# Optimization experiments

Measured on AMD Instinct MI355X. Metric: run time of the kernel, lower is better.

Reference implementation:

```python
import jax, jax.numpy as jnp
import numpy as np

TOP_K = 4
NUM_EXPERTS = 128
HIDDEN_DIM = 2880


def setup_inputs() -> dict:
    key = jax.random.key(0)
    k1, k2, k3 = jax.random.split(key, 3)
    hidden_states = jax.random.normal(k1, (4, 4096, HIDDEN_DIM), dtype=jnp.float32)
    weight = jax.random.normal(k2, (NUM_EXPERTS, HIDDEN_DIM), dtype=jnp.float32) * 0.02
    bias = jax.random.normal(k3, (NUM_EXPERTS,), dtype=jnp.float32) * 0.02
    return {"hidden_states": hidden_states, "weight": weight, "bias": bias}


def reference(hidden_states, weight, bias):
    # flatten tokens: [T, H]
    h = hidden_states.reshape(-1, HIDDEN_DIM)
    # router logits: [T, E]
    router_logits = jnp.einsum("th,eh->te", h, weight) + bias
    # top-k over experts
    router_top_value, router_indices = jax.lax.top_k(router_logits, TOP_K)  # [T, K]
    # softmax over the k selected logits only
    router_top_value = jax.nn.softmax(router_top_value, axis=-1)
    # scatter softmaxed weights back into dense [T, E] score matrix
    T = router_logits.shape[0]
    rows = jnp.arange(T)[:, None]  # [T, 1] broadcast against [T, K]
    router_scores = jnp.zeros_like(router_logits).at[rows, router_indices].set(router_top_value)
    # histogram of expert selections
    expert_select_count = jnp.zeros((NUM_EXPERTS,), dtype=jnp.int32).at[router_indices.reshape(-1)].add(
        jnp.ones((T * TOP_K,), dtype=jnp.int32)
    )
    return router_scores, router_indices, expert_select_count
```

## Files before the change

kernel.cpp:

```cpp
#include <hip/hip_runtime.h>
#include <math.h>

#define HID 2880
#define NE  128
#define BK  64
#define TOKB 64
#define NCH 45
#define HN  15
#define PSTR 129

typedef _Float16 half4v __attribute__((ext_vector_type(4)));
typedef _Float16 half8v __attribute__((ext_vector_type(8)));
typedef float    f32x4v __attribute__((ext_vector_type(4)));

__global__ __launch_bounds__(256)
void prep_w(const float* __restrict__ W, _Float16* __restrict__ whi,
            _Float16* __restrict__ wlo)
{
    const int e = blockIdx.x;
    for (int j = 0; j < 12; ++j) {
        const int k = j * 256 + threadIdx.x;
        if (k >= HID) break;
        const float v = W[(size_t)e * HID + k];
        const _Float16 h = (_Float16)v;
        const _Float16 l = (_Float16)(v - (float)h);
        const size_t idx = (size_t)(k >> 6) * 8192 + ((k >> 5) & 1) * 4096
                         + e * 32 + (k & 31);
        whi[idx] = h;
        wlo[idx] = l;
    }
}

#define GLOAD(dst, ptr) \
    asm volatile("global_load_dwordx4 %0, %1, off" : "=v"(dst) : "v"(ptr))

__global__ __launch_bounds__(768, 1)
void fused_router(const float* __restrict__ A, const _Float16* __restrict__ whi,
                  const _Float16* __restrict__ wlo, const float* __restrict__ bias,
                  float* __restrict__ scores, float* __restrict__ idxOut,
                  float* __restrict__ counts)
{
    __shared__ __align__(16) char smem[98304];
    __shared__ float sval[TOKB][4];
    __shared__ int   sidx[TOKB][4];
    __shared__ int   hist[NE];

#define SA(ks, buf, h, sub) \
    (smem + (ks) * 32768 + ((((buf) * 2 + (h)) * 2 + (sub)) * 4096))

#define SWZ(tok) ((((tok) >> 1) & 3) << 4)

    const int tid  = threadIdx.x;
    const int lane = tid & 63;
    const int wv   = __builtin_amdgcn_readfirstlane(tid >> 6);
    const int ks   = wv >> 2;
    const int wq   = wv & 3;
    const int lg   = lane >> 4;
    const int lr   = lane & 15;
    const int tokBase = blockIdx.x * TOKB;
    const int hbeg = ks * HN;

    const _Float16* wHp[2];
    const _Float16* wLp[2];
#pragma unroll
    for (int m = 0; m < 2; ++m) {
        const size_t b = (size_t)((wq * 32 + m * 16 + lr) * 32 + lg * 8);
        wHp[m] = whi + b;
        wLp[m] = wlo + b;
    }

    const int gid = tid & 255;
    const float* aSrcP[4];
    int aSub[4], aWr[4];
#pragma unroll
    for (int p = 0; p < 4; ++p) {
        const int f = p * 256 + gid;
        const int tok = f >> 4, sl = f & 15;
        aSub[p] = sl >> 3;
        const int q = sl & 7;
        aSrcP[p] = A + (size_t)(tokBase + tok) * HID + aSub[p] * 32 + q * 4;
        aWr[p] = tok * 64 + ((q * 8) ^ SWZ(tok));
    }

    int aRd[4];
#pragma unroll
    for (int n = 0; n < 4; ++n) {
        const int tok = n * 16 + lr;
        aRd[n] = tok * 64 + ((lg * 16) ^ SWZ(tok));
    }

    float4 aA, aB, aC, aD;
#define AISSUE(c) do {                                                         \
    GLOAD(aA, aSrcP[0] + (size_t)(c) * BK);                                    \
    GLOAD(aB, aSrcP[1] + (size_t)(c) * BK);                                    \
    GLOAD(aC, aSrcP[2] + (size_t)(c) * BK);                                    \
    GLOAD(aD, aSrcP[3] + (size_t)(c) * BK);                                    \
} while (0)

#define WISSUE(SET, c) do {                                                    \
    _Pragma("unroll")                                                          \
    for (int m = 0; m < 2; ++m)                                                \
        _Pragma("unroll")                                                      \
        for (int s = 0; s < 2; ++s) {                                          \
            const size_t o = (size_t)(c) * 8192 + s * 4096;                    \
            GLOAD(SET[m * 4 + s * 2 + 0], wHp[m] + o);                         \
            GLOAD(SET[m * 4 + s * 2 + 1], wLp[m] + o);                         \
        }                                                                      \
} while (0)

    auto CONVA = [&](int buf) {
#pragma unroll
        for (int p = 0; p < 4; ++p) {
            const float4 v = (p == 0) ? aA : (p == 1) ? aB : (p == 2) ? aC : aD;
            const _Float16 h0 = (_Float16)v.x, h1 = (_Float16)v.y,
                           h2 = (_Float16)v.z, h3 = (_Float16)v.w;
            const half4v hh = {h0, h1, h2, h3};
            const half4v ll = {(_Float16)(v.x - (float)h0),
                               (_Float16)(v.y - (float)h1),
                               (_Float16)(v.z - (float)h2),
                               (_Float16)(v.w - (float)h3)};
            *reinterpret_cast<half4v*>(SA(ks, buf, 0, aSub[p]) + aWr[p]) = hh;
            *reinterpret_cast<half4v*>(SA(ks, buf, 1, aSub[p]) + aWr[p]) = ll;
        }
    };

    f32x4v acc[2][4];
#pragma unroll
    for (int m = 0; m < 2; ++m)
#pragma unroll
        for (int n = 0; n < 4; ++n) acc[m][n] = (f32x4v)0.f;

    half8v wA[8], wB[8];

#define STEP(i, SU, SF) do {                                                   \
    if ((i) + 1 < HN) { AISSUE(hbeg + (i) + 1); WISSUE(SF, hbeg + (i) + 1); }  \
    __builtin_amdgcn_sched_barrier(0);                                         \
    if ((i) + 1 < HN) asm volatile("s_waitcnt vmcnt(12)" ::: "memory");        \
    else              asm volatile("s_waitcnt vmcnt(0)" ::: "memory");         \
    __builtin_amdgcn_sched_barrier(0);                                         \
    const int buf_ = (i) & 1;                                                  \
    _Pragma("unroll")                                                          \
    for (int s = 0; s < 2; ++s)                                                \
        _Pragma("unroll")                                                      \
        for (int n = 0; n < 4; ++n) {                                          \
            const half8v ah = *reinterpret_cast<const half8v*>(                \
                SA(ks, buf_, 0, s) + aRd[n]);                                  \
            const half8v al = *reinterpret_cast<const half8v*>(                \
                SA(ks, buf_, 1, s) + aRd[n]);                                  \
            _Pragma("unroll")                                                  \
            for (int m = 0; m < 2; ++m) {                                      \
                acc[m][n] = __builtin_amdgcn_mfma_f32_16x16x32_f16(            \
                    SU[m * 4 + s * 2 + 0], ah, acc[m][n], 0, 0, 0);            \
                acc[m][n] = __builtin_amdgcn_mfma_f32_16x16x32_f16(            \
                    SU[m * 4 + s * 2 + 1], ah, acc[m][n], 0, 0, 0);            \
                acc[m][n] = __builtin_amdgcn_mfma_f32_16x16x32_f16(            \
                    SU[m * 4 + s * 2 + 0], al, acc[m][n], 0, 0, 0);            \
            }                                                                  \
        }                                                                      \
    if ((i) + 1 < HN) {                                                        \
        asm volatile("s_waitcnt vmcnt(8)" ::: "memory");                       \
        __builtin_amdgcn_sched_barrier(0);                                     \
        CONVA(((i) + 1) & 1);                                                  \
    }                                                                          \
    asm volatile("s_waitcnt lgkmcnt(0)" ::: "memory");                         \
    __builtin_amdgcn_sched_barrier(0);                                         \
    __builtin_amdgcn_s_barrier();                                              \
    __builtin_amdgcn_sched_barrier(0);                                         \
} while (0)

    AISSUE(hbeg);
    WISSUE(wA, hbeg);
    asm volatile("s_waitcnt vmcnt(8)" ::: "memory");
    __builtin_amdgcn_sched_barrier(0);
    CONVA(0);
    asm volatile("s_waitcnt lgkmcnt(0)" ::: "memory");
    __builtin_amdgcn_sched_barrier(0);
    __builtin_amdgcn_s_barrier();
    __builtin_amdgcn_sched_barrier(0);

#pragma unroll 1
    for (int i = 0; i < HN - 1; i += 2) {
        STEP(i,     wA, wB);
        STEP(i + 1, wB, wA);
    }
    STEP(HN - 1, wA, wB);

    float* P1   = (float*)(smem);
    float* P2   = (float*)(smem + 33024);
    float* cval = (float*)(smem + 66048);
    int*   cidx = (int*)(smem + 74496);

    if (tid < NE) hist[tid] = 0;

    if (ks == 1 || ks == 2) {
        float* P = (ks == 1) ? P1 : P2;
#pragma unroll
        for (int m = 0; m < 2; ++m)
#pragma unroll
            for (int n = 0; n < 4; ++n)
#pragma unroll
                for (int r = 0; r < 4; ++r) {
                    const int e = wq * 32 + m * 16 + lg * 4 + r;
                    const int t = n * 16 + lr;
                    P[t * PSTR + e] = acc[m][n][r];
                }
    }
    __syncthreads();

    if (ks == 0) {
#pragma unroll
        for (int m = 0; m < 2; ++m)
#pragma unroll
            for (int n = 0; n < 4; ++n)
#pragma unroll
                for (int r = 0; r < 4; ++r) {
                    const int e = wq * 32 + m * 16 + lg * 4 + r;
                    const int t = n * 16 + lr;
                    const int off = t * PSTR + e;
                    P1[off] = ((acc[m][n][r] + P1[off]) + P2[off]) + bias[e];
                }
    }
    __syncthreads();

    if (tid < 512) {
        const int t = tid & 63, g = tid >> 6;
        float v0 = -1e30f, v1 = -1e30f, v2 = -1e30f, v3 = -1e30f;
        int   i0 = 0, i1 = 0, i2 = 0, i3 = 0;
        const int e0 = g * 16;
#pragma unroll 4
        for (int i = 0; i < 16; ++i) {
            const int e = e0 + i;
            const float v = P1[t * PSTR + e];
            if (v > v3) {
                if (v > v2) {
                    v3 = v2; i3 = i2;
                    if (v > v1) {
                        v2 = v1; i2 = i1;
                        if (v > v0) { v1 = v0; i1 = i0; v0 = v; i0 = e; }
                        else        { v1 = v;  i1 = e; }
                    } else { v2 = v; i2 = e; }
                } else { v3 = v; i3 = e; }
            }
        }
        cval[t * 33 + g * 4 + 0] = v0; cidx[t * 33 + g * 4 + 0] = i0;
        cval[t * 33 + g * 4 + 1] = v1; cidx[t * 33 + g * 4 + 1] = i1;
        cval[t * 33 + g * 4 + 2] = v2; cidx[t * 33 + g * 4 + 2] = i2;
        cval[t * 33 + g * 4 + 3] = v3; cidx[t * 33 + g * 4 + 3] = i3;
    }
    __syncthreads();

    if (tid < TOKB) {
        const int t = tid;
        float m0 = -1e30f, m1 = -1e30f, m2 = -1e30f, m3 = -1e30f;
        int   j0 = 0, j1 = 0, j2 = 0, j3 = 0;
#pragma unroll
        for (int q = 0; q < 32; ++q) {
            const float v = cval[t * 33 + q];
            const int   e = cidx[t * 33 + q];
            if (v > m3) {
                if (v > m2) {
                    m3 = m2; j3 = j2;
                    if (v > m1) {
                        m2 = m1; j2 = j1;
                        if (v > m0) { m1 = m0; j1 = j0; m0 = v; j0 = e; }
                        else        { m1 = v;  j1 = e; }
                    } else { m2 = v; j2 = e; }
                } else { m3 = v; j3 = e; }
            }
        }
        const float x1 = expf(m1 - m0), x2 = expf(m2 - m0), x3 = expf(m3 - m0);
        const float inv = 1.f / (1.f + x1 + x2 + x3);
        sval[t][0] = inv;      sidx[t][0] = j0;
        sval[t][1] = x1 * inv; sidx[t][1] = j1;
        sval[t][2] = x2 * inv; sidx[t][2] = j2;
        sval[t][3] = x3 * inv; sidx[t][3] = j3;
        atomicAdd(&hist[j0], 1); atomicAdd(&hist[j1], 1);
        atomicAdd(&hist[j2], 1); atomicAdd(&hist[j3], 1);
    }
    __syncthreads();

    const size_t sBase = (size_t)blockIdx.x * TOKB * NE;
#pragma unroll 4
    for (int it = 0; it < 11; ++it) {
        const int flat = it * 768 + tid;
        if (flat < TOKB * NE) {
            const int t = flat >> 7, e = flat & 127;
            float val = 0.f;
            val = (e == sidx[t][0]) ? sval[t][0] : val;
            val = (e == sidx[t][1]) ? sval[t][1] : val;
            val = (e == sidx[t][2]) ? sval[t][2] : val;
            val = (e == sidx[t][3]) ? sval[t][3] : val;
            scores[sBase + flat] = val;
        }
    }
    if (tid < TOKB * 4)
        idxOut[(size_t)blockIdx.x * TOKB * 4 + tid] =
            (float)sidx[tid >> 2][tid & 3];
    if (tid < NE) {
        const int c = hist[tid];
        if (c) atomicAdd(&counts[tid], (float)c);
    }
#undef SA
#undef SWZ
#undef AISSUE
#undef WISSUE
#undef STEP
}

extern "C" void kernel_launch(void* const* d_in, const int* in_sizes, int n_in,
                              void* d_out, int out_size, void* d_ws, size_t ws_size,
                              hipStream_t stream) {
    const float* A = (const float*)d_in[0];
    const float* W = (const float*)d_in[1];
    const float* B = (const float*)d_in[2];
    const int T = in_sizes[0] / HID;

    float* out = (float*)d_out;
    float* scores = out;
    float* idxOut = out + (size_t)T * NE;
    float* counts = idxOut + (size_t)T * 4;

    _Float16* whi = (_Float16*)d_ws;
    _Float16* wlo = whi + (size_t)NE * HID;

    hipMemsetAsync(counts, 0, NE * sizeof(float), stream);

    hipLaunchKernelGGL(prep_w, dim3(NE), dim3(256), 0, stream, W, whi, wlo);
    hipLaunchKernelGGL(fused_router, dim3(T / TOKB), dim3(768), 0, stream,
                       A, whi, wlo, B, scores, idxOut, counts);
}
```

Measured before the change: 65.38 us.

## Halve token and K tiles to cut LDS and registers for multi-block occupancy

Reduces the per-block token tile from 64 to 32 and the K chunk from 64 to 32. This shrinks shared memory from about 96KB to about 41KB and halves the accumulator and weight register sets, and launch bounds now request 6 blocks per CU instead of 1. The load pipeline, address math, vmcnt thresholds, LDS layout and top-k/scatter loops are all reworked to match. The intent is more resident blocks and waves to hide memory latency and to spread 512 blocks instead of 256 across CUs. The cost is that every weight chunk is reloaded twice as often per token, and each step carries more pipeline and synchronisation overhead.

```diff
diff --git a/kernel.cpp b/kernel.cpp
--- a/kernel.cpp
+++ b/kernel.cpp
@@ -3,10 +3,10 @@
 
 #define HID 2880
 #define NE  128
-#define BK  64
-#define TOKB 64
-#define NCH 45
-#define HN  15
+#define BK  32
+#define TOKB 32
+#define NCH 90
+#define HN  30
 #define PSTR 129
 
 typedef _Float16 half4v __attribute__((ext_vector_type(4)));
@@ -33,20 +33,22 @@
 
 #define GLOAD(dst, ptr) \
     asm volatile("global_load_dwordx4 %0, %1, off" : "=v"(dst) : "v"(ptr))
-
-__global__ __launch_bounds__(768, 1)
+#define GLOAD_O1024(dst, ptr) \
+    asm volatile("global_load_dwordx4 %0, %1, off offset:1024" : "=v"(dst) : "v"(ptr))
+
+__global__ __launch_bounds__(768, 6)
 void fused_router(const float* __restrict__ A, const _Float16* __restrict__ whi,
                   const _Float16* __restrict__ wlo, const float* __restrict__ bias,
                   float* __restrict__ scores, float* __restrict__ idxOut,
                   float* __restrict__ counts)
 {
-    __shared__ __align__(16) char smem[98304];
+    __shared__ __align__(16) char smem[41472];
     __shared__ float sval[TOKB][4];
     __shared__ int   sidx[TOKB][4];
     __shared__ int   hist[NE];
 
-#define SA(ks, buf, h, sub) \
-    (smem + (ks) * 32768 + ((((buf) * 2 + (h)) * 2 + (sub)) * 4096))
+#define SA(ks, buf, h) \
+    (smem + (ks) * 8192 + (((buf) * 2 + (h)) * 2048))
 
 #define SWZ(tok) ((((tok) >> 1) & 3) << 4)
 
@@ -60,105 +62,79 @@
     const int tokBase = blockIdx.x * TOKB;
     const int hbeg = ks * HN;
 
-    const _Float16* wHp[2];
-    const _Float16* wLp[2];
-#pragma unroll
-    for (int m = 0; m < 2; ++m) {
-        const size_t b = (size_t)((wq * 32 + m * 16 + lr) * 32 + lg * 8);
-        wHp[m] = whi + b;
-        wLp[m] = wlo + b;
-    }
+    const _Float16* wHp0 = whi + (size_t)((wq * 32 + lr) * 32 + lg * 8);
+    const _Float16* wLp0 = wlo + (size_t)((wq * 32 + lr) * 32 + lg * 8);
 
     const int gid = tid & 255;
-    const float* aSrcP[4];
-    int aSub[4], aWr[4];
-#pragma unroll
-    for (int p = 0; p < 4; ++p) {
-        const int f = p * 256 + gid;
-        const int tok = f >> 4, sl = f & 15;
-        aSub[p] = sl >> 3;
-        const int q = sl & 7;
-        aSrcP[p] = A + (size_t)(tokBase + tok) * HID + aSub[p] * 32 + q * 4;
-        aWr[p] = tok * 64 + ((q * 8) ^ SWZ(tok));
-    }
-
-    int aRd[4];
-#pragma unroll
-    for (int n = 0; n < 4; ++n) {
+    const int ptok = gid >> 3, pq = gid & 7;
+    const float* aSrc = A + (size_t)(tokBase + ptok) * HID + pq * 4;
+    const int aWr = ptok * 64 + ((pq * 8) ^ SWZ(ptok));
+
+    int aRd[2];
+#pragma unroll
+    for (int n = 0; n < 2; ++n) {
         const int tok = n * 16 + lr;
         aRd[n] = tok * 64 + ((lg * 16) ^ SWZ(tok));
     }
 
-    float4 aA, aB, aC, aD;
-#define AISSUE(c) do {                                                         \
-    GLOAD(aA, aSrcP[0] + (size_t)(c) * BK);                                    \
-    GLOAD(aB, aSrcP[1] + (size_t)(c) * BK);                                    \
-    GLOAD(aC, aSrcP[2] + (size_t)(c) * BK);                                    \
-    GLOAD(aD, aSrcP[3] + (size_t)(c) * BK);                                    \
+    float4 aA;
+#define AISSUE(c) GLOAD(aA, aSrc + (size_t)(c) * BK)
+
+#define WISSUE(SET, c) do {                                                    \
+    const _Float16* hp_ = wHp0 + (size_t)(c) * 4096;                           \
+    const _Float16* lp_ = wLp0 + (size_t)(c) * 4096;                           \
+    GLOAD(SET[0], hp_);                                                        \
+    GLOAD(SET[1], lp_);                                                        \
+    GLOAD_O1024(SET[2], hp_);                                                  \
+    GLOAD_O1024(SET[3], lp_);                                                  \
 } while (0)
 
-#define WISSUE(SET, c) do {                                                    \
-    _Pragma("unroll")                                                          \
-    for (int m = 0; m < 2; ++m)                                                \
-        _Pragma("unroll")                                                      \
-        for (int s = 0; s < 2; ++s) {                                          \
-            const size_t o = (size_t)(c) * 8192 + s * 4096;                    \
-            GLOAD(SET[m * 4 + s * 2 + 0], wHp[m] + o);                         \
-            GLOAD(SET[m * 4 + s * 2 + 1], wLp[m] + o);                         \
-        }                                                                      \
-} while (0)
-
     auto CONVA = [&](int buf) {
-#pragma unroll
-        for (int p = 0; p < 4; ++p) {
-            const float4 v = (p == 0) ? aA : (p == 1) ? aB : (p == 2) ? aC : aD;
-            const _Float16 h0 = (_Float16)v.x, h1 = (_Float16)v.y,
-                           h2 = (_Float16)v.z, h3 = (_Float16)v.w;
-            const half4v hh = {h0, h1, h2, h3};
-            const half4v ll = {(_Float16)(v.x - (float)h0),
-                               (_Float16)(v.y - (float)h1),
-                               (_Float16)(v.z - (float)h2),
-                               (_Float16)(v.w - (float)h3)};
-            *reinterpret_cast<half4v*>(SA(ks, buf, 0, aSub[p]) + aWr[p]) = hh;
-            *reinterpret_cast<half4v*>(SA(ks, buf, 1, aSub[p]) + aWr[p]) = ll;
-        }
+        const float4 v = aA;
+        const _Float16 h0 = (_Float16)v.x, h1 = (_Float16)v.y,
+                       h2 = (_Float16)v.z, h3 = (_Float16)v.w;
+        const half4v hh = {h0, h1, h2, h3};
+        const half4v ll = {(_Float16)(v.x - (float)h0),
+                           (_Float16)(v.y - (float)h1),
+                           (_Float16)(v.z - (float)h2),
+                           (_Float16)(v.w - (float)h3)};
+        *reinterpret_cast<half4v*>(SA(ks, buf, 0) + aWr) = hh;
+        *reinterpret_cast<half4v*>(SA(ks, buf, 1) + aWr) = ll;
     };
 
-    f32x4v acc[2][4];
+    f32x4v acc[2][2];
 #pragma unroll
     for (int m = 0; m < 2; ++m)
 #pragma unroll
-        for (int n = 0; n < 4; ++n) acc[m][n] = (f32x4v)0.f;
-
-    half8v wA[8], wB[8];
+        for (int n = 0; n < 2; ++n) acc[m][n] = (f32x4v)0.f;
+
+    half8v wA[4], wB[4];
 
 #define STEP(i, SU, SF) do {                                                   \
     if ((i) + 1 < HN) { AISSUE(hbeg + (i) + 1); WISSUE(SF, hbeg + (i) + 1); }  \
     __builtin_amdgcn_sched_barrier(0);                                         \
-    if ((i) + 1 < HN) asm volatile("s_waitcnt vmcnt(12)" ::: "memory");        \
+    if ((i) + 1 < HN) asm volatile("s_waitcnt vmcnt(5)" ::: "memory");         \
     else              asm volatile("s_waitcnt vmcnt(0)" ::: "memory");         \
     __builtin_amdgcn_sched_barrier(0);                                         \
     const int buf_ = (i) & 1;                                                  \
     _Pragma("unroll")                                                          \
-    for (int s = 0; s < 2; ++s)                                                \
+    for (int n = 0; n < 2; ++n) {                                              \
+        const half8v ah = *reinterpret_cast<const half8v*>(                    \
+            SA(ks, buf_, 0) + aRd[n]);                                         \
+        const half8v al = *reinterpret_cast<const half8v*>(                    \
+            SA(ks, buf_, 1) + aRd[n]);                                         \
         _Pragma("unroll")                                                      \
-        for (int n = 0; n < 4; ++n) {                                          \
-            const half8v ah = *reinterpret_cast<const half8v*>(                \
-                SA(ks, buf_, 0, s) + aRd[n]);                                  \
-            const half8v al = *reinterpret_cast<const half8v*>(                \
-                SA(ks, buf_, 1, s) + aRd[n]);                                  \
-            _Pragma("unroll")                                                  \
-            for (int m = 0; m < 2; ++m) {                                      \
-                acc[m][n] = __builtin_amdgcn_mfma_f32_16x16x32_f16(            \
-                    SU[m * 4 + s * 2 + 0], ah, acc[m][n], 0, 0, 0);            \
-                acc[m][n] = __builtin_amdgcn_mfma_f32_16x16x32_f16(            \
-                    SU[m * 4 + s * 2 + 1], ah, acc[m][n], 0, 0, 0);            \
-                acc[m][n] = __builtin_amdgcn_mfma_f32_16x16x32_f16(            \
-                    SU[m * 4 + s * 2 + 0], al, acc[m][n], 0, 0, 0);            \
-            }                                                                  \
+        for (int m = 0; m < 2; ++m) {                                          \
+            acc[m][n] = __builtin_amdgcn_mfma_f32_16x16x32_f16(                \
+                SU[m * 2 + 0], ah, acc[m][n], 0, 0, 0);                        \
+            acc[m][n] = __builtin_amdgcn_mfma_f32_16x16x32_f16(                \
+                SU[m * 2 + 1], ah, acc[m][n], 0, 0, 0);                        \
+            acc[m][n] = __builtin_amdgcn_mfma_f32_16x16x32_f16(                \
+                SU[m * 2 + 0], al, acc[m][n], 0, 0, 0);                        \
         }                                                                      \
+    }                                                                          \
     if ((i) + 1 < HN) {                                                        \
-        asm volatile("s_waitcnt vmcnt(8)" ::: "memory");                       \
+        asm volatile("s_waitcnt vmcnt(4)" ::: "memory");                       \
         __builtin_amdgcn_sched_barrier(0);                                     \
         CONVA(((i) + 1) & 1);                                                  \
     }                                                                          \
@@ -170,7 +146,7 @@
 
     AISSUE(hbeg);
     WISSUE(wA, hbeg);
-    asm volatile("s_waitcnt vmcnt(8)" ::: "memory");
+    asm volatile("s_waitcnt vmcnt(4)" ::: "memory");
     __builtin_amdgcn_sched_barrier(0);
     CONVA(0);
     asm volatile("s_waitcnt lgkmcnt(0)" ::: "memory");
@@ -179,16 +155,15 @@
     __builtin_amdgcn_sched_barrier(0);
 
 #pragma unroll 1
-    for (int i = 0; i < HN - 1; i += 2) {
+    for (int i = 0; i < HN; i += 2) {
         STEP(i,     wA, wB);
         STEP(i + 1, wB, wA);
     }
-    STEP(HN - 1, wA, wB);
 
     float* P1   = (float*)(smem);
-    float* P2   = (float*)(smem + 33024);
-    float* cval = (float*)(smem + 66048);
-    int*   cidx = (int*)(smem + 74496);
+    float* P2   = (float*)(smem + 16512);
+    float* cval = (float*)(smem + 33024);
+    int*   cidx = (int*)(smem + 37248);
 
     if (tid < NE) hist[tid] = 0;
 
@@ -197,7 +172,7 @@
 #pragma unroll
         for (int m = 0; m < 2; ++m)
 #pragma unroll
-            for (int n = 0; n < 4; ++n)
+            for (int n = 0; n < 2; ++n)
 #pragma unroll
                 for (int r = 0; r < 4; ++r) {
                     const int e = wq * 32 + m * 16 + lg * 4 + r;
@@ -211,7 +186,7 @@
 #pragma unroll
         for (int m = 0; m < 2; ++m)
 #pragma unroll
-            for (int n = 0; n < 4; ++n)
+            for (int n = 0; n < 2; ++n)
 #pragma unroll
                 for (int r = 0; r < 4; ++r) {
                     const int e = wq * 32 + m * 16 + lg * 4 + r;
@@ -222,8 +197,8 @@
     }
     __syncthreads();
 
-    if (tid < 512) {
-        const int t = tid & 63, g = tid >> 6;
+    if (tid < 256) {
+        const int t = tid & 31, g = tid >> 5;
         float v0 = -1e30f, v1 = -1e30f, v2 = -1e30f, v3 = -1e30f;
         int   i0 = 0, i1 = 0, i2 = 0, i3 = 0;
         const int e0 = g * 16;
@@ -280,8 +255,8 @@
     __syncthreads();
 
     const size_t sBase = (size_t)blockIdx.x * TOKB * NE;
-#pragma unroll 4
-    for (int it = 0; it < 11; ++it) {
+#pragma unroll 3
+    for (int it = 0; it < 6; ++it) {
         const int flat = it * 768 + tid;
         if (flat < TOKB * NE) {
             const int t = flat >> 7, e = flat & 127;
```

Measured after the change: 82.39 us. 1.26x slower.

## Split K-reduction across separate blocks with partials in global memory and a reduce kernel

Applied to the files above, without the earlier changes.

The single 768-thread block, which split the hidden dimension three ways and reduced in shared memory, becomes three independent 256-thread blocks per token tile. Each block writes its partial logits to global buffers (one of them the scores output), and a new reduce kernel sums them, adds bias, and does top-k, softmax, scatter and histogram. The aim is more blocks and better occupancy, with smaller LDS and three blocks per CU. In exchange it adds an extra launch and a global round-trip of three T×128 float partial buffers.

```diff
diff --git a/kernel.cpp b/kernel.cpp
--- a/kernel.cpp
+++ b/kernel.cpp
@@ -5,7 +5,6 @@
 #define NE  128
 #define BK  64
 #define TOKB 64
-#define NCH 45
 #define HN  15
 #define PSTR 129
 
@@ -34,30 +33,25 @@
 #define GLOAD(dst, ptr) \
     asm volatile("global_load_dwordx4 %0, %1, off" : "=v"(dst) : "v"(ptr))
 
-__global__ __launch_bounds__(768, 1)
+__global__ __launch_bounds__(256, 3)
 void fused_router(const float* __restrict__ A, const _Float16* __restrict__ whi,
-                  const _Float16* __restrict__ wlo, const float* __restrict__ bias,
-                  float* __restrict__ scores, float* __restrict__ idxOut,
-                  float* __restrict__ counts)
+                  const _Float16* __restrict__ wlo, float* __restrict__ p0,
+                  float* __restrict__ p1, float* __restrict__ p2)
 {
-    __shared__ __align__(16) char smem[98304];
-    __shared__ float sval[TOKB][4];
-    __shared__ int   sidx[TOKB][4];
-    __shared__ int   hist[NE];
-
-#define SA(ks, buf, h, sub) \
-    (smem + (ks) * 32768 + ((((buf) * 2 + (h)) * 2 + (sub)) * 4096))
-
+    __shared__ __align__(16) char smem[32768];
+
+#define SA(buf, h, sub) (smem + ((((buf) * 2 + (h)) * 2 + (sub)) * 4096))
 #define SWZ(tok) ((((tok) >> 1) & 3) << 4)
 
     const int tid  = threadIdx.x;
     const int lane = tid & 63;
-    const int wv   = __builtin_amdgcn_readfirstlane(tid >> 6);
-    const int ks   = wv >> 2;
-    const int wq   = wv & 3;
+    const int wq   = __builtin_amdgcn_readfirstlane(tid >> 6);
+    const int bid  = blockIdx.x;
+    const int ks   = bid % 3;
+    const int tb   = bid / 3;
     const int lg   = lane >> 4;
     const int lr   = lane & 15;
-    const int tokBase = blockIdx.x * TOKB;
+    const int tokBase = tb * TOKB;
     const int hbeg = ks * HN;
 
     const _Float16* wHp[2];
@@ -69,16 +63,15 @@
         wLp[m] = wlo + b;
     }
 
-    const int gid = tid & 255;
     const float* aSrcP[4];
     int aSub[4], aWr[4];
 #pragma unroll
     for (int p = 0; p < 4; ++p) {
-        const int f = p * 256 + gid;
+        const int f = p * 256 + tid;
         const int tok = f >> 4, sl = f & 15;
         aSub[p] = sl >> 3;
         const int q = sl & 7;
-        aSrcP[p] = A + (size_t)(tokBase + tok) * HID + aSub[p] * 32 + q * 4;
+        aSrcP[p] = A + (size_t)(tokBase + tok) * HID + ks * 960 + aSub[p] * 32 + q * 4;
         aWr[p] = tok * 64 + ((q * 8) ^ SWZ(tok));
     }
 
@@ -119,8 +112,8 @@
                                (_Float16)(v.y - (float)h1),
                                (_Float16)(v.z - (float)h2),
                                (_Float16)(v.w - (float)h3)};
-            *reinterpret_cast<half4v*>(SA(ks, buf, 0, aSub[p]) + aWr[p]) = hh;
-            *reinterpret_cast<half4v*>(SA(ks, buf, 1, aSub[p]) + aWr[p]) = ll;
+            *reinterpret_cast<half4v*>(SA(buf, 0, aSub[p]) + aWr[p]) = hh;
+            *reinterpret_cast<half4v*>(SA(buf, 1, aSub[p]) + aWr[p]) = ll;
         }
     };
 
@@ -133,7 +126,7 @@
     half8v wA[8], wB[8];
 
 #define STEP(i, SU, SF) do {                                                   \
-    if ((i) + 1 < HN) { AISSUE(hbeg + (i) + 1); WISSUE(SF, hbeg + (i) + 1); }  \
+    if ((i) + 1 < HN) { AISSUE((i) + 1); WISSUE(SF, hbeg + (i) + 1); }         \
     __builtin_amdgcn_sched_barrier(0);                                         \
     if ((i) + 1 < HN) asm volatile("s_waitcnt vmcnt(12)" ::: "memory");        \
     else              asm volatile("s_waitcnt vmcnt(0)" ::: "memory");         \
@@ -144,9 +137,9 @@
         _Pragma("unroll")                                                      \
         for (int n = 0; n < 4; ++n) {                                          \
             const half8v ah = *reinterpret_cast<const half8v*>(                \
-                SA(ks, buf_, 0, s) + aRd[n]);                                  \
+                SA(buf_, 0, s) + aRd[n]);                                      \
             const half8v al = *reinterpret_cast<const half8v*>(                \
-                SA(ks, buf_, 1, s) + aRd[n]);                                  \
+                SA(buf_, 1, s) + aRd[n]);                                      \
             _Pragma("unroll")                                                  \
             for (int m = 0; m < 2; ++m) {                                      \
                 acc[m][n] = __builtin_amdgcn_mfma_f32_16x16x32_f16(            \
@@ -168,7 +161,7 @@
     __builtin_amdgcn_sched_barrier(0);                                         \
 } while (0)
 
-    AISSUE(hbeg);
+    AISSUE(0);
     WISSUE(wA, hbeg);
     asm volatile("s_waitcnt vmcnt(8)" ::: "memory");
     __builtin_amdgcn_sched_barrier(0);
@@ -185,44 +178,51 @@
     }
     STEP(HN - 1, wA, wB);
 
-    float* P1   = (float*)(smem);
-    float* P2   = (float*)(smem + 33024);
-    float* cval = (float*)(smem + 66048);
-    int*   cidx = (int*)(smem + 74496);
+    float* P = (ks == 0) ? p0 : (ks == 1) ? p1 : p2;
+#pragma unroll
+    for (int m = 0; m < 2; ++m)
+#pragma unroll
+        for (int n = 0; n < 4; ++n) {
+            const int e = wq * 32 + m * 16 + lg * 4;
+            const int t = n * 16 + lr;
+            *reinterpret_cast<f32x4v*>(
+                &P[(size_t)(tokBase + t) * NE + e]) = acc[m][n];
+        }
+#undef SA
+#undef SWZ
+#undef AISSUE
+#undef WISSUE
+#undef STEP
+}
+
+__global__ __launch_bounds__(512)
+void reduce_router(float* __restrict__ scores, const float* __restrict__ p1,
+                   const float* __restrict__ p2, const float* __restrict__ bias,
+                   float* __restrict__ idxOut, float* __restrict__ counts)
+{
+    __shared__ float P[TOKB * PSTR];
+    __shared__ float cval[TOKB * 33];
+    __shared__ int   cidx[TOKB * 33];
+    __shared__ float sval[TOKB][4];
+    __shared__ int   sidx[TOKB][4];
+    __shared__ int   hist[NE];
+
+    const int tid = threadIdx.x;
+    const int tb  = blockIdx.x;
+    const size_t base = (size_t)tb * TOKB * NE;
 
     if (tid < NE) hist[tid] = 0;
 
-    if (ks == 1 || ks == 2) {
-        float* P = (ks == 1) ? P1 : P2;
-#pragma unroll
-        for (int m = 0; m < 2; ++m)
-#pragma unroll
-            for (int n = 0; n < 4; ++n)
-#pragma unroll
-                for (int r = 0; r < 4; ++r) {
-                    const int e = wq * 32 + m * 16 + lg * 4 + r;
-                    const int t = n * 16 + lr;
-                    P[t * PSTR + e] = acc[m][n][r];
-                }
+#pragma unroll
+    for (int it = 0; it < 16; ++it) {
+        const int flat = it * 512 + tid;
+        const int t = flat >> 7, e = flat & 127;
+        P[t * PSTR + e] = ((scores[base + flat] + p1[base + flat])
+                           + p2[base + flat]) + bias[e];
     }
     __syncthreads();
 
-    if (ks == 0) {
-#pragma unroll
-        for (int m = 0; m < 2; ++m)
-#pragma unroll
-            for (int n = 0; n < 4; ++n)
-#pragma unroll
-                for (int r = 0; r < 4; ++r) {
-                    const int e = wq * 32 + m * 16 + lg * 4 + r;
-                    const int t = n * 16 + lr;
-                    const int off = t * PSTR + e;
-                    P1[off] = ((acc[m][n][r] + P1[off]) + P2[off]) + bias[e];
-                }
-    }
-    __syncthreads();
-
-    if (tid < 512) {
+    {
         const int t = tid & 63, g = tid >> 6;
         float v0 = -1e30f, v1 = -1e30f, v2 = -1e30f, v3 = -1e30f;
         int   i0 = 0, i1 = 0, i2 = 0, i3 = 0;
@@ -230,7 +230,7 @@
 #pragma unroll 4
         for (int i = 0; i < 16; ++i) {
             const int e = e0 + i;
-            const float v = P1[t * PSTR + e];
+            const float v = P[t * PSTR + e];
             if (v > v3) {
                 if (v > v2) {
                     v3 = v2; i3 = i2;
@@ -279,32 +279,23 @@
     }
     __syncthreads();
 
-    const size_t sBase = (size_t)blockIdx.x * TOKB * NE;
-#pragma unroll 4
-    for (int it = 0; it < 11; ++it) {
-        const int flat = it * 768 + tid;
-        if (flat < TOKB * NE) {
-            const int t = flat >> 7, e = flat & 127;
-            float val = 0.f;
-            val = (e == sidx[t][0]) ? sval[t][0] : val;
-            val = (e == sidx[t][1]) ? sval[t][1] : val;
-            val = (e == sidx[t][2]) ? sval[t][2] : val;
-            val = (e == sidx[t][3]) ? sval[t][3] : val;
-            scores[sBase + flat] = val;
-        }
+#pragma unroll
+    for (int it = 0; it < 16; ++it) {
+        const int flat = it * 512 + tid;
+        const int t = flat >> 7, e = flat & 127;
+        float val = 0.f;
+        val = (e == sidx[t][0]) ? sval[t][0] : val;
+        val = (e == sidx[t][1]) ? sval[t][1] : val;
+        val = (e == sidx[t][2]) ? sval[t][2] : val;
+        val = (e == sidx[t][3]) ? sval[t][3] : val;
+        scores[base + flat] = val;
     }
     if (tid < TOKB * 4)
-        idxOut[(size_t)blockIdx.x * TOKB * 4 + tid] =
-            (float)sidx[tid >> 2][tid & 3];
+        idxOut[(size_t)tb * TOKB * 4 + tid] = (float)sidx[tid >> 2][tid & 3];
     if (tid < NE) {
         const int c = hist[tid];
         if (c) atomicAdd(&counts[tid], (float)c);
     }
-#undef SA
-#undef SWZ
-#undef AISSUE
-#undef WISSUE
-#undef STEP
 }
 
 extern "C" void kernel_launch(void* const* d_in, const int* in_sizes, int n_in,
@@ -322,10 +313,14 @@
 
     _Float16* whi = (_Float16*)d_ws;
     _Float16* wlo = whi + (size_t)NE * HID;
+    float* p1 = (float*)(wlo + (size_t)NE * HID);
+    float* p2 = p1 + (size_t)T * NE;
 
     hipMemsetAsync(counts, 0, NE * sizeof(float), stream);
 
     hipLaunchKernelGGL(prep_w, dim3(NE), dim3(256), 0, stream, W, whi, wlo);
-    hipLaunchKernelGGL(fused_router, dim3(T / TOKB), dim3(768), 0, stream,
-                       A, whi, wlo, B, scores, idxOut, counts);
+    hipLaunchKernelGGL(fused_router, dim3((T / TOKB) * 3), dim3(256), 0, stream,
+                       A, whi, wlo, scores, p1, p2);
+    hipLaunchKernelGGL(reduce_router, dim3(T / TOKB), dim3(512), 0, stream,
+                       scores, p1, p2, B, idxOut, counts);
 }
```

Measured after the change: 74.55 us. 1.14x slower.
